# Optimization experiments

Hardware: AMD Instinct MI355X
Metric: run time of the kernel (lower is better)

Reference implementation:

```python
import jax, jax.numpy as jnp
import numpy as np

B, S, D = 4, 8192, 768
H, HD = 12, 64
CS, NL = 512, 32


def setup_inputs() -> dict:
    key = jax.random.key(0)
    ks = jax.random.split(key, 9)
    sc = 0.02
    return {
        "x": jax.random.normal(ks[0], (B, S, D), jnp.float32),
        "q_w": jax.random.normal(ks[1], (D, D), jnp.float32) * sc,
        "q_b": jax.random.normal(ks[2], (D,), jnp.float32) * sc,
        "k_w": jax.random.normal(ks[3], (D, D), jnp.float32) * sc,
        "k_b": jax.random.normal(ks[4], (D,), jnp.float32) * sc,
        "v_w": jax.random.normal(ks[5], (D, D), jnp.float32) * sc,
        "v_b": jax.random.normal(ks[6], (D,), jnp.float32) * sc,
        "o_w": jax.random.normal(ks[7], (D, D), jnp.float32) * sc,
        "o_b": jax.random.normal(ks[8], (D,), jnp.float32) * sc,
    }


def reference(x, q_w, q_b, k_w, k_b, v_w, v_b, o_w, o_b):
    # x: (B, S, D); S divisible by CS and NL -> no padding / trimming needed.
    scale = HD ** -0.5
    n_chunks = S // CS
    seg = S // NL
    # Global landmarks: mean-pool NL evenly spaced segments. (B, NL, D)
    landmarks = x.reshape(B, NL, seg, D).mean(axis=2)
    # Q only over local tokens (torch Linear: x @ W^T + b)
    q = (x @ q_w.T + q_b).reshape(B, n_chunks, CS, H, HD)
    x_chunks = x.reshape(B, n_chunks, CS, D)
    # Prepend landmarks to every chunk's KV context: ctx = NL + CS
    lm = jnp.broadcast_to(landmarks[:, None], (B, n_chunks, NL, D))
    kv_ctx = jnp.concatenate([lm, x_chunks], axis=2)  # (B, n_chunks, ctx, D)
    ctx = NL + CS
    k = (kv_ctx @ k_w.T + k_b).reshape(B, n_chunks, ctx, H, HD)
    v = (kv_ctx @ v_w.T + v_b).reshape(B, n_chunks, ctx, H, HD)
    scores = jnp.einsum("bnqhd,bnkhd->bnhqk", q, k) * scale
    attn = jax.nn.softmax(scores, axis=-1)  # dropout=0 (eval)
    out = jnp.einsum("bnhqk,bnkhd->bnqhd", attn, v).reshape(B, S, D)
    return out @ o_w.T + o_b
```

## Files before the change

### kernel.cpp

```cpp
#include <hip/hip_runtime.h>


typedef unsigned short u16;
typedef __attribute__((ext_vector_type(8))) short short8;
typedef __attribute__((ext_vector_type(4))) float f32x4;

__device__ __forceinline__ u16 f2bf(float f) {
    unsigned u = __float_as_uint(f);
    u += 0x7fffu + ((u >> 16) & 1u);
    return (u16)(u >> 16);
}

#define MFMA_BF16(A, B, C) __builtin_amdgcn_mfma_f32_16x16x32_bf16((A), (B), (C), 0, 0, 0)

__device__ __forceinline__ void gload16(const u16* g, const short* l) {
    __builtin_amdgcn_global_load_lds(
        (__attribute__((address_space(1))) void*)g,
        (__attribute__((address_space(3))) void*)l, 16, 0, 0);
}

__global__ __launch_bounds__(256) void k_cvtx(const float* __restrict__ x,
                                              u16* __restrict__ xa,
                                              float* __restrict__ part2) {
    const int g = blockIdx.x;
    const int t = threadIdx.x, q = t >> 6, l = t & 63;
    const float* base = x + (size_t)g * 64 * 768;
    u16* ob = xa + (size_t)g * 64 * 768;
    float s[3][4] = {};
    for (int it = 0; it < 16; ++it) {
        const size_t ro = (size_t)(it * 4 + q) * 768;
#pragma unroll
        for (int k = 0; k < 3; ++k) {
            const int c4 = (l + k * 64) * 4;
            const float4 v = *(const float4*)(base + ro + c4);
            s[k][0] += v.x; s[k][1] += v.y; s[k][2] += v.z; s[k][3] += v.w;
            ushort4 o;
            o.x = f2bf(v.x); o.y = f2bf(v.y); o.z = f2bf(v.z); o.w = f2bf(v.w);
            *(ushort4*)(ob + ro + c4) = o;
        }
    }
    float* p = part2 + (size_t)(g * 4 + q) * 768;
#pragma unroll
    for (int k = 0; k < 3; ++k)
#pragma unroll
        for (int j = 0; j < 4; ++j)
            p[(l + k * 64) * 4 + j] = s[k][j];
}

__global__ void k_lmred(const float* __restrict__ part2, u16* __restrict__ xa_lm) {
    const int bl = blockIdx.x;
    const int t = threadIdx.x;
    const float* p = part2 + (size_t)bl * 16 * 768;
    const float inv = 1.f / 256.f;
    for (int c = t; c < 768; c += 256) {
        float s = 0.f;
#pragma unroll
        for (int i = 0; i < 16; ++i) s += p[i * 768 + c];
        xa_lm[(size_t)bl * 768 + c] = f2bf(s * inv);
    }
}

#define QSCALE 0.1803368801111243f

__global__ void k_cvtw(const float* __restrict__ qw, const float* __restrict__ kw,
                       const float* __restrict__ vw, const float* __restrict__ ow,
                       const float* __restrict__ qb, const float* __restrict__ kb,
                       const float* __restrict__ vb,
                       u16* __restrict__ wcat, u16* __restrict__ owb,
                       float* __restrict__ bcat) {
    const int yy = blockIdx.y;
    const int i = blockIdx.x * 256 + threadIdx.x;
    if (yy == 4) {
        if (i < 768)       bcat[i] = qb[i] * QSCALE;
        else if (i < 1536) bcat[i] = kb[i - 768];
        else if (i < 2304) bcat[i] = vb[i - 1536];
        return;
    }
    const float* src = (yy == 0) ? qw : (yy == 1) ? kw : (yy == 2) ? vw : ow;
    u16* dst = (yy == 3) ? owb : wcat + (size_t)yy * 589824;
    const float scl = (yy == 0) ? QSCALE : 1.0f;
    const float4 v = ((const float4*)src)[i];
    ushort4 o;
    o.x = f2bf(v.x * scl); o.y = f2bf(v.y * scl);
    o.z = f2bf(v.z * scl); o.w = f2bf(v.w * scl);
    ((ushort4*)dst)[i] = o;
}

template <int MODE>
__global__ __launch_bounds__(512, 4) void k_gemm(
    const u16* __restrict__ A, const u16* __restrict__ Bw, const float* __restrict__ bias,
    u16* __restrict__ qx, u16* __restrict__ ktok, u16* __restrict__ vt,
    u16* __restrict__ klm, u16* __restrict__ vlmt, float* __restrict__ outf)
{
    __shared__ short lA[2][4096];
    __shared__ short lB[2][8192];
    const int t = threadIdx.x;
    const int wid = t >> 6, lane = t & 63, lr = lane & 15, lg = lane >> 4;
    const int wm = wid >> 2, wn = wid & 3;

    const int gx = gridDim.x;
    const int nwg = gx * gridDim.y;
    const int orig = blockIdx.x + gx * blockIdx.y;
    const int qq = nwg >> 3, rr = nwg & 7, xcd = orig & 7, ii = orig >> 3;
    const int wg = (xcd < rr ? xcd * (qq + 1) : rr * (qq + 1) + (xcd - rr) * qq) + ii;
    const int m0 = (wg / gx) * 128, n0 = (wg % gx) * 256;

    const int rA = t >> 2,        cA = ((t & 3) ^ ((rA >> 1) & 3)) * 8;
    const int uB1 = 512 + t;
    const int rB1 = uB1 >> 2,     cB1 = ((uB1 & 3) ^ ((rB1 >> 1) & 3)) * 8;
    const u16* pa0 = A  + (size_t)(m0 + rA) * 768 + cA;
    const u16* pb0 = Bw + (size_t)(n0 + rA) * 768 + cA;
    const u16* pb1 = Bw + (size_t)(n0 + rB1) * 768 + cB1;
    const int sa = (lg ^ ((lr >> 1) & 3)) * 8;

#define STG(S, T) {                                            \
    gload16(pa0 + (T) * 32, &lA[S][wid * 512]);                \
    gload16(pb0 + (T) * 32, &lB[S][wid * 512]);                \
    gload16(pb1 + (T) * 32, &lB[S][4096 + wid * 512]); }

    f32x4 acc[4][4] = {};
    STG(0, 0); STG(1, 1);

#pragma unroll
    for (int T = 0; T < 24; ++T) {
        const int s = T & 1;
        if (T < 23) asm volatile("s_waitcnt vmcnt(3)" ::: "memory");
        else        asm volatile("s_waitcnt vmcnt(0)" ::: "memory");
        __builtin_amdgcn_s_barrier();
        __builtin_amdgcn_sched_barrier(0);
        short8 aq[4], bq[4];
#pragma unroll
        for (int mf = 0; mf < 4; ++mf)
            aq[mf] = *(const short8*)&lA[s][(wm * 64 + mf * 16 + lr) * 32 + sa];
#pragma unroll
        for (int nf = 0; nf < 4; ++nf)
            bq[nf] = *(const short8*)&lB[s][(wn * 64 + nf * 16 + lr) * 32 + sa];
        asm volatile("s_waitcnt lgkmcnt(0)" ::: "memory");
        __builtin_amdgcn_sched_barrier(0);
        __builtin_amdgcn_s_barrier();
        if (T + 2 < 24) STG(s, T + 2);
        __builtin_amdgcn_s_setprio(1);
#pragma unroll
        for (int mf = 0; mf < 4; ++mf)
#pragma unroll
            for (int nf = 0; nf < 4; ++nf)
                acc[mf][nf] = MFMA_BF16(aq[mf], bq[nf], acc[mf][nf]);
        __builtin_amdgcn_s_setprio(0);
    }
#undef STG

    if (MODE == 0) {
        const int region = n0 / 768;
        if (region == 2) {
#pragma unroll
            for (int nf = 0; nf < 4; ++nf) {
                const int gn = n0 + wn * 64 + nf * 16 + lr;
                const float bv = bias[gn];
                const int nn = gn - 1536;
                const int h = nn >> 6, d = nn & 63;
#pragma unroll
                for (int mf = 0; mf < 4; ++mf) {
                    const int gmb = m0 + wm * 64 + mf * 16 + lg * 4;
                    ushort4 w;
                    w.x = f2bf(acc[mf][nf][0] + bv);
                    w.y = f2bf(acc[mf][nf][1] + bv);
                    w.z = f2bf(acc[mf][nf][2] + bv);
                    w.w = f2bf(acc[mf][nf][3] + bv);
                    if (gmb < 32768) {
                        const int b = gmb >> 13, ss = gmb & 8191;
                        *(ushort4*)(vt + ((size_t)(b * 12 + h) * 64 + d) * 8192 + ss) = w;
                    } else {
                        const int ii2 = gmb - 32768;
                        const int bb = ii2 >> 5, lmr = ii2 & 31;
                        *(ushort4*)(vlmt + ((size_t)(bb * 12 + h) * 64 + d) * 32 + lmr) = w;
                    }
                }
            }
        } else {
            u16* dst = (region == 0) ? qx : ktok;
#pragma unroll
            for (int nf = 0; nf < 4; ++nf) {
                const int gn = n0 + wn * 64 + nf * 16 + lr;
                const int nn = gn - region * 768;
                const int h = nn >> 6, d = nn & 63;
                const float bv = bias[gn];
#pragma unroll
                for (int mf = 0; mf < 4; ++mf) {
                    const int gmb = m0 + wm * 64 + mf * 16 + lg * 4;
#pragma unroll
                    for (int r = 0; r < 4; ++r) {
                        const int gm = gmb + r;
                        const u16 val = f2bf(acc[mf][nf][r] + bv);
                        if (gm < 32768) {
                            const int b = gm >> 13, ss = gm & 8191;
                            dst[((size_t)(b * 12 + h) * 8192 + ss) * 64 + d] = val;
                        } else if (region == 1) {
                            const int ii2 = gm - 32768;
                            klm[((size_t)((ii2 >> 5) * 12 + h) * 32 + (ii2 & 31)) * 64 + d] = val;
                        }
                    }
                }
            }
        }
    } else {
#pragma unroll
        for (int nf = 0; nf < 4; ++nf) {
            const int gn = n0 + wn * 64 + nf * 16 + lr;
            const float bvv = bias[gn];
#pragma unroll
            for (int mf = 0; mf < 4; ++mf) {
                const int gmb = m0 + wm * 64 + mf * 16 + lg * 4;
#pragma unroll
                for (int r = 0; r < 4; ++r)
                    outf[(size_t)(gmb + r) * 768 + gn] = acc[mf][nf][r] + bvv;
            }
        }
    }
}

__global__ __launch_bounds__(256) void k_attn(
    const u16* __restrict__ q, const u16* __restrict__ ktok,
    const u16* __restrict__ klm, const u16* __restrict__ vt,
    const u16* __restrict__ vlmt, u16* __restrict__ ao)
{
    __shared__ short kls[2][32 * 72];
    __shared__ short vls[2][64 * 40];
    __shared__ short pls[4][64 * 40];
    const int t = threadIdx.x, wid = t >> 6, l = t & 63, lr = l & 15, lg = l >> 4;
    const int idx = blockIdx.x;
    const int qt = idx & 1;
    const int h  = (idx >> 1) % 12;
    const int cb = (idx >> 1) / 12;
    const int c  = cb & 15, b = cb >> 4;
    const int bh = b * 12 + h;
    const int sb = c * 512 + qt * 256 + wid * 64;

    short8 qf[4][2];
#pragma unroll
    for (int mf = 0; mf < 4; ++mf)
#pragma unroll
        for (int kf = 0; kf < 2; ++kf)
            qf[mf][kf] = *(const short8*)(q + ((size_t)bh * 8192 + sb + mf * 16 + lr) * 64
                                            + kf * 32 + lg * 8);

    f32x4 O[4][5] = {};
    const short8 vones = {0x3F80, 0x3F80, 0x3F80, 0x3F80,
                          0x3F80, 0x3F80, 0x3F80, 0x3F80};

    short* pw = &pls[wid][0];
    const int kn = t >> 3, kko = (t & 7) * 8;
    const int kctx = (kn < 16) ? (kn * 2) : ((kn - 16) * 2 + 1);
    const int vd = t >> 2, vco = (t & 3) * 8;

    auto kaddr = [&](int ti) -> const u16* {
        if (ti == 0) return klm + ((size_t)bh * 32 + kctx) * 64 + kko;
        return ktok + ((size_t)bh * 8192 + c * 512 + (ti - 1) * 32 + kctx) * 64 + kko;
    };
    auto vaddr = [&](int ti) -> const u16* {
        if (ti == 0) return vlmt + ((size_t)bh * 64 + vd) * 32 + vco;
        return vt + ((size_t)bh * 64 + vd) * 8192 + c * 512 + (ti - 1) * 32 + vco;
    };

    {
        const uint4 rk0 = *(const uint4*)kaddr(0);
        const uint4 rv0 = *(const uint4*)vaddr(0);
        *(uint4*)&kls[0][kn * 72 + kko] = rk0;
        *(uint4*)&vls[0][vd * 40 + vco] = rv0;
    }
    __syncthreads();

    for (int ti = 0; ti < 17; ++ti) {
        const int cur = ti & 1, nxt = cur ^ 1;
        uint4 rk, rv;
        if (ti < 16) { rk = *(const uint4*)kaddr(ti + 1); rv = *(const uint4*)vaddr(ti + 1); }

        f32x4 sc[4][2] = {};
        __builtin_amdgcn_s_setprio(1);
#pragma unroll
        for (int kf = 0; kf < 2; ++kf) {
            const short8 b0 = *(const short8*)&kls[cur][(lr)      * 72 + kf * 32 + lg * 8];
            const short8 b1 = *(const short8*)&kls[cur][(16 + lr) * 72 + kf * 32 + lg * 8];
#pragma unroll
            for (int mf = 0; mf < 4; ++mf) {
                sc[mf][0] = MFMA_BF16(qf[mf][kf], b0, sc[mf][0]);
                sc[mf][1] = MFMA_BF16(qf[mf][kf], b1, sc[mf][1]);
            }
        }
        __builtin_amdgcn_s_setprio(0);

#pragma unroll
        for (int mf = 0; mf < 4; ++mf) {
#pragma unroll
            for (int r = 0; r < 4; ++r) {
                const float p0 = exp2f(sc[mf][0][r]);
                const float p1 = exp2f(sc[mf][1][r]);
                unsigned pk;
                asm("v_cvt_pk_bf16_f32 %0, %1, %2" : "=v"(pk) : "v"(p0), "v"(p1));
                const int prow = mf * 16 + lg * 4 + r;
                ((unsigned*)pw)[prow * 20 + lr] = pk;
            }
        }

        short8 vb[4];
#pragma unroll
        for (int df = 0; df < 4; ++df)
            vb[df] = *(const short8*)&vls[cur][(df * 16 + lr) * 40 + lg * 8];
        __builtin_amdgcn_s_setprio(1);
#pragma unroll
        for (int mf = 0; mf < 4; ++mf) {
            const short8 pa2 = *(const short8*)&pw[(mf * 16 + lr) * 40 + lg * 8];
#pragma unroll
            for (int df = 0; df < 4; ++df)
                O[mf][df] = MFMA_BF16(pa2, vb[df], O[mf][df]);
            O[mf][4] = MFMA_BF16(pa2, vones, O[mf][4]);
        }
        __builtin_amdgcn_s_setprio(0);

        if (ti < 16) {
            *(uint4*)&kls[nxt][kn * 72 + kko] = rk;
            *(uint4*)&vls[nxt][vd * 40 + vco] = rv;
        }
        __syncthreads();
    }

#pragma unroll
    for (int mf = 0; mf < 4; ++mf)
#pragma unroll
        for (int r = 0; r < 4; ++r) {
            const float inv = 1.f / O[mf][4][r];
            const int srow = sb + mf * 16 + lg * 4 + r;
#pragma unroll
            for (int df = 0; df < 4; ++df)
                ao[((size_t)b * 8192 + srow) * 768 + h * 64 + df * 16 + lr] =
                    f2bf(O[mf][df][r] * inv);
        }
}

extern "C" void kernel_launch(void* const* d_in, const int* in_sizes, int n_in,
                              void* d_out, int out_size, void* d_ws, size_t ws_size,
                              hipStream_t stream)
{
    const float* x  = (const float*)d_in[0];
    const float* qw = (const float*)d_in[1];
    const float* qb = (const float*)d_in[2];
    const float* kw = (const float*)d_in[3];
    const float* kb = (const float*)d_in[4];
    const float* vw = (const float*)d_in[5];
    const float* vb = (const float*)d_in[6];
    const float* ow = (const float*)d_in[7];
    const float* ob = (const float*)d_in[8];
    float* out = (float*)d_out;

    u16* xa     = (u16*)d_ws;
    u16* wcat   = xa + (size_t)32896 * 768;
    u16* owb    = wcat + (size_t)2304 * 768;
    float* bcat = (float*)(owb + (size_t)768 * 768);
    u16* qx     = (u16*)(bcat + 2304);
    u16* ktok   = qx   + (size_t)32768 * 768;
    u16* vt     = ktok + (size_t)32768 * 768;
    u16* klm    = vt + (size_t)32768 * 768;
    u16* vlmt   = klm + 98304;
    float* part2= (float*)(vlmt + 98304);
    u16* ao     = xa;

    k_cvtx<<<512, 256, 0, stream>>>(x, xa, part2);
    k_lmred<<<128, 256, 0, stream>>>(part2, xa + (size_t)32768 * 768);
    k_cvtw<<<dim3(576, 5), 256, 0, stream>>>(qw, kw, vw, ow, qb, kb, vb, wcat, owb, bcat);

    k_gemm<0><<<dim3(9, 257), 512, 0, stream>>>(xa, wcat, bcat,
                                                qx, ktok, vt, klm, vlmt, nullptr);
    k_attn<<<1536, 256, 0, stream>>>(qx, ktok, klm, vt, vlmt, ao);
    k_gemm<1><<<dim3(3, 256), 512, 0, stream>>>(ao, owb, ob,
                                                nullptr, nullptr, nullptr, nullptr, nullptr, out);
}
```

Before: 354.9 us.

## Deepen K/V register prefetch to two tiles ahead in attention loop

```diff
diff --git a/kernel.cpp b/kernel.cpp
--- a/kernel.cpp
+++ b/kernel.cpp
@@ -218,7 +218,7 @@
     }
 }
 
-__global__ __launch_bounds__(256) void k_attn(
+__global__ __launch_bounds__(256, 3) void k_attn(
     const u16* __restrict__ q, const u16* __restrict__ ktok,
     const u16* __restrict__ klm, const u16* __restrict__ vt,
     const u16* __restrict__ vlmt, u16* __restrict__ ao)
@@ -261,18 +261,19 @@
         return vt + ((size_t)bh * 64 + vd) * 8192 + c * 512 + (ti - 1) * 32 + vco;
     };
 
-    {
-        const uint4 rk0 = *(const uint4*)kaddr(0);
-        const uint4 rv0 = *(const uint4*)vaddr(0);
-        *(uint4*)&kls[0][kn * 72 + kko] = rk0;
-        *(uint4*)&vls[0][vd * 40 + vco] = rv0;
-    }
-    __syncthreads();
-
+    uint4 rk[2], rv[2];
+    rk[0] = *(const uint4*)kaddr(0); rv[0] = *(const uint4*)vaddr(0);
+    rk[1] = *(const uint4*)kaddr(1); rv[1] = *(const uint4*)vaddr(1);
+    *(uint4*)&kls[0][kn * 72 + kko] = rk[0];
+    *(uint4*)&vls[0][vd * 40 + vco] = rv[0];
+    rk[0] = *(const uint4*)kaddr(2); rv[0] = *(const uint4*)vaddr(2);
+    asm volatile("s_waitcnt lgkmcnt(0)" ::: "memory");
+    __builtin_amdgcn_sched_barrier(0);
+    __builtin_amdgcn_s_barrier();
+
+#pragma unroll
     for (int ti = 0; ti < 17; ++ti) {
         const int cur = ti & 1, nxt = cur ^ 1;
-        uint4 rk, rv;
-        if (ti < 16) { rk = *(const uint4*)kaddr(ti + 1); rv = *(const uint4*)vaddr(ti + 1); }
 
         f32x4 sc[4][2] = {};
         __builtin_amdgcn_s_setprio(1);
@@ -317,10 +318,14 @@
         __builtin_amdgcn_s_setprio(0);
 
         if (ti < 16) {
-            *(uint4*)&kls[nxt][kn * 72 + kko] = rk;
-            *(uint4*)&vls[nxt][vd * 40 + vco] = rv;
-        }
-        __syncthreads();
+            *(uint4*)&kls[nxt][kn * 72 + kko] = rk[nxt];
+            *(uint4*)&vls[nxt][vd * 40 + vco] = rv[nxt];
+            if (ti + 3 < 17) { rk[nxt] = *(const uint4*)kaddr(ti + 3);
+                               rv[nxt] = *(const uint4*)vaddr(ti + 3); }
+            asm volatile("s_waitcnt lgkmcnt(0)" ::: "memory");
+            __builtin_amdgcn_sched_barrier(0);
+            __builtin_amdgcn_s_barrier();
+        }
     }
 
 #pragma unroll
```

Measured after the change: 626.2 us. +76.4%, slower.
